# Kernel optimization log

Hardware: AMD Instinct MI355X
Metric: run time of the kernel (lower is better)

Reference implementation:

```python
import jax, jax.numpy as jnp
import numpy as np

K = 12  # Emb.k: piece-type planes (6 types x 2 colors)
DOUT = 256
B = 16384          # number of positions (bags)
AVG_LEN = 30       # avg active features per position
T = B * AVG_LEN    # total ragged ids
S = (1.0 / 30.0) ** 0.5  # 1/sqrt(kRoughEstimateOfNumberOfOnesInInput)

# vertical board flip permutation over the 64 king squares
_SQ = np.arange(64)
_FLIP_PERM = jnp.asarray((7 - _SQ // 8) * 8 + _SQ % 8)


def _flip_vertical(x):
    # x: [64, K, 8, 8, d] -> flip ranks, swap color planes, flip king square
    x = jnp.flip(x, axis=2)
    x = jnp.roll(x, K // 2, axis=1)
    return x[_FLIP_PERM]


def setup_inputs() -> dict:
    key = jax.random.key(0)
    ks = jax.random.split(key, 8)
    pieces = jax.random.normal(ks[0], (64, K, 1, 1, DOUT), dtype=jnp.float32) * S
    ranks = jax.random.normal(ks[1], (64, K, 8, 1, DOUT), dtype=jnp.float32) * S
    files = jax.random.normal(ks[2], (64, K, 1, 8, DOUT), dtype=jnp.float32) * S
    tiles = jax.random.normal(ks[3], (64, K, 8, 8, DOUT), dtype=jnp.float32) * S
    mask = jnp.ones((64, K, 8, 8, 1), dtype=jnp.float32)
    mask = (mask.at[:, 0, 0, :, :].set(0.0)
                .at[:, 0, 7, :, :].set(0.0)
                .at[:, K // 2, 0, :, :].set(0.0)
                .at[:, K // 2, 7, :, :].set(0.0))
    # ragged lengths that sum exactly to T: antithetic pairs around AVG_LEN
    half = B // 2
    d = jax.random.randint(ks[4], (half,), -10, 11)
    lengths = jnp.concatenate([AVG_LEN + d, AVG_LEN - d]).astype(jnp.int64)
    values = jax.random.randint(ks[5], (T,), 0, K * 64).astype(jnp.int64)
    kings = jax.random.randint(ks[6], (B, 2), 0, 64).astype(jnp.int64)
    return dict(pieces=pieces, ranks=ranks, files=files, tiles=tiles,
                factorization_mask=mask, values=values, lengths=lengths, kings=kings)


def reference(pieces, ranks, files, tiles, factorization_mask, values, lengths, kings):
    # factorized merge: [64, K, 8, 8, d]
    merged = tiles + (pieces + ranks + files) * factorization_mask
    d = merged.shape[-1]
    w = merged.reshape(64 * K * 64, d)
    flipped = _flip_vertical(merged).reshape(64 * K * 64, d)

    n_bags = lengths.shape[0]
    total = values.shape[0]
    # segment id for each ragged element (== repeat_interleave of bag index)
    seg = jnp.repeat(jnp.arange(n_bags), lengths, total_repeat_length=total)
    piece_dim = K * 64
    mover_ids = kings[seg, 0] * piece_dim + values
    waiter_ids = kings[seg, 1] * piece_dim + values

    a = jax.ops.segment_sum(w[mover_ids], seg, num_segments=n_bags)
    b = jax.ops.segment_sum(flipped[waiter_ids], seg, num_segments=n_bags)
    return jnp.clip(a, 0.0, 1.0), jnp.clip(b, 0.0, 1.0)
```

## Files before the change

### kernel.cpp

```cpp
#include <hip/hip_runtime.h>

#define DOUT 256
#define NROWS 49152
#define MATB (NROWS / 16)

__device__ __forceinline__ float4 ld4(const float* p) {
  return *reinterpret_cast<const float4*>(p);
}

__device__ __forceinline__ unsigned rne2(float a, float b) {
  unsigned ua = __float_as_uint(a), ub = __float_as_uint(b);
  ua += 0x7FFFu + ((ua >> 16) & 1u);
  ub += 0x7FFFu + ((ub >> 16) & 1u);
  return (ua >> 16) | (ub & 0xFFFF0000u);
}

__device__ __forceinline__ void bf4_acc(uint2 w, float4& acc) {
  acc.x += __uint_as_float(w.x << 16);
  acc.y += __uint_as_float(w.x & 0xFFFF0000u);
  acc.z += __uint_as_float(w.y << 16);
  acc.w += __uint_as_float(w.y & 0xFFFF0000u);
}

__global__ __launch_bounds__(1024) void prep_kernel(
    const float* __restrict__ tiles, const float* __restrict__ pieces,
    const float* __restrict__ ranks, const float* __restrict__ files,
    const float* __restrict__ mask, uint2* __restrict__ merged,
    const int* __restrict__ lengths, const int* __restrict__ kings,
    int* __restrict__ offs, int* __restrict__ perm_m, int* __restrict__ perm_w,
    int n_bags) {
  const int bid = blockIdx.x;
  const int t = threadIdx.x;
  if (bid == 0) {
    __shared__ int part[1024];
    __shared__ int histM[64], histW[64], curW[64];
    const int nb = n_bags;
    int v[16];
    const int base = t * 16;
    int s = 0;
    if (base + 16 <= nb) {
#pragma unroll
      for (int j = 0; j < 16; j += 4) {
        const int4 x = *reinterpret_cast<const int4*>(lengths + base + j);
        v[j] = x.x; v[j + 1] = x.y; v[j + 2] = x.z; v[j + 3] = x.w;
      }
#pragma unroll
      for (int j = 0; j < 16; ++j) s += v[j];
    } else {
      for (int j = 0; j < 16; ++j) {
        const int idx = base + j;
        v[j] = (idx < nb) ? lengths[idx] : 0;
        s += v[j];
      }
    }
    part[t] = s;
    __syncthreads();
    for (int off = 1; off < 1024; off <<= 1) {
      const int w = (t >= off) ? part[t - off] : 0;
      __syncthreads();
      part[t] += w;
      __syncthreads();
    }
    int run = part[t] - s;
    for (int j = 0; j < 16; ++j) {
      const int idx = base + j;
      if (idx < nb) { offs[idx] = run; run += v[j]; }
    }
    if (t < 64) { histM[t] = 0; histW[t] = 0; }
    __syncthreads();
    for (int i = t; i < nb; i += 1024) {
      const int2 kk = *reinterpret_cast<const int2*>(kings + 2 * i);
      atomicAdd(&histM[kk.x], 1);
      atomicAdd(&histW[kk.y], 1);
    }
    __syncthreads();
    if (t == 0) {
      int r = 0;
      for (int k = 0; k < 64; ++k) { const int h = histM[k]; histM[k] = r; r += h; }
    }
    if (t == 1) {
      int r = 0;
      for (int k = 0; k < 64; ++k) { curW[k] = r; r += histW[k]; }
    }
    __syncthreads();
    for (int i = t; i < nb; i += 1024) {
      const int2 kk = *reinterpret_cast<const int2*>(kings + 2 * i);
      const int pm = atomicAdd(&histM[kk.x], 1);
      perm_m[pm] = i;
      const int pw = atomicAdd(&curW[kk.y], 1);
      perm_w[pw] = i;
    }
    return;
  }
  const int row = ((bid - 1) << 4) + (t >> 6);
  const int lane = t & 63;
  const int p = row & 63;
  const int sk = row >> 6;
  const int r = p >> 3, f = p & 7;
  const float m = mask[row];
  const int d0 = lane << 2;
  const float4 tl = ld4(tiles + (size_t)row * DOUT + d0);
  const float4 pc = ld4(pieces + (size_t)sk * DOUT + d0);
  const float4 rk = ld4(ranks + (size_t)(sk * 8 + r) * DOUT + d0);
  const float4 fl = ld4(files + (size_t)(sk * 8 + f) * DOUT + d0);
  float4 o;
  o.x = fmaf(pc.x + rk.x + fl.x, m, tl.x);
  o.y = fmaf(pc.y + rk.y + fl.y, m, tl.y);
  o.z = fmaf(pc.z + rk.z + fl.z, m, tl.z);
  o.w = fmaf(pc.w + rk.w + fl.w, m, tl.w);
  uint2 w;
  w.x = rne2(o.x, o.y);
  w.y = rne2(o.z, o.w);
  merged[(size_t)row * 64 + lane] = w;
}

template <bool WAITER>
__device__ __forceinline__ void gather_body(
    const uint2* __restrict__ merged, const int* __restrict__ values,
    const int* __restrict__ lengths, const int* __restrict__ kings,
    const int* __restrict__ offs, const int* __restrict__ perm,
    float* __restrict__ out, int n_bags, int chunk, int b) {
  const int c = b & 7;
  const int j = b >> 3;
  const int pos = c * chunk + (j << 2) + (threadIdx.x >> 6);
  const int lim = min((c + 1) * chunk, n_bags);
  if (pos >= lim) return;
  const int lane = threadIdx.x & 63;
  const int bag = perm[pos];
  const int len = lengths[bag];
  const int kg = kings[2 * bag + (WAITER ? 1 : 0)];
  const int base = (WAITER ? (((7 - (kg >> 3)) << 3) + (kg & 7)) : kg) * 768;
  const int* __restrict__ vals = values + offs[bag];
  const uint2* __restrict__ mb = merged + lane;

  float4 a0 = {0.f, 0.f, 0.f, 0.f}, a1 = {0.f, 0.f, 0.f, 0.f};

  int i = 0;
  for (; i + 4 <= len; i += 4) {
    const int v0 = vals[i], v1 = vals[i + 1], v2 = vals[i + 2], v3 = vals[i + 3];
    unsigned r0, r1, r2, r3;
    if (WAITER) {
      const int k0 = v0 >> 6, k1 = v1 >> 6, k2 = v2 >> 6, k3 = v3 >> 6;
      r0 = base + ((k0 < 6 ? k0 + 6 : k0 - 6) << 6) + ((v0 & 63) ^ 56);
      r1 = base + ((k1 < 6 ? k1 + 6 : k1 - 6) << 6) + ((v1 & 63) ^ 56);
      r2 = base + ((k2 < 6 ? k2 + 6 : k2 - 6) << 6) + ((v2 & 63) ^ 56);
      r3 = base + ((k3 < 6 ? k3 + 6 : k3 - 6) << 6) + ((v3 & 63) ^ 56);
    } else {
      r0 = base + v0; r1 = base + v1; r2 = base + v2; r3 = base + v3;
    }
    const uint2 x0 = mb[(size_t)r0 << 6];
    const uint2 x1 = mb[(size_t)r1 << 6];
    const uint2 x2 = mb[(size_t)r2 << 6];
    const uint2 x3 = mb[(size_t)r3 << 6];
    bf4_acc(x0, a0); bf4_acc(x1, a1); bf4_acc(x2, a0); bf4_acc(x3, a1);
  }
  for (; i < len; ++i) {
    const int v = vals[i];
    unsigned r;
    if (WAITER) {
      const int k = v >> 6;
      r = base + ((k < 6 ? k + 6 : k - 6) << 6) + ((v & 63) ^ 56);
    } else {
      r = base + v;
    }
    bf4_acc(mb[(size_t)r << 6], a0);
  }

  float4 o;
  o.x = fminf(fmaxf(a0.x + a1.x, 0.f), 1.f);
  o.y = fminf(fmaxf(a0.y + a1.y, 0.f), 1.f);
  o.z = fminf(fmaxf(a0.z + a1.z, 0.f), 1.f);
  o.w = fminf(fmaxf(a0.w + a1.w, 0.f), 1.f);
  float4* ob = reinterpret_cast<float4*>(out) +
               (WAITER ? (size_t)n_bags * 64 : 0);
  ob[(size_t)bag * 64 + lane] = o;
}

__global__ __launch_bounds__(256) void gather_kernel(
    const uint2* __restrict__ merged, const int* __restrict__ values,
    const int* __restrict__ lengths, const int* __restrict__ kings,
    const int* __restrict__ offs, const int* __restrict__ perm_m,
    const int* __restrict__ perm_w, float* __restrict__ out, int n_bags,
    int chunk, int half_blocks) {
  const int b = blockIdx.x;
  if (b < half_blocks) {
    gather_body<false>(merged, values, lengths, kings, offs, perm_m, out,
                       n_bags, chunk, b);
  } else {
    gather_body<true>(merged, values, lengths, kings, offs, perm_w, out,
                      n_bags, chunk, b - half_blocks);
  }
}

extern "C" void kernel_launch(void* const* d_in, const int* in_sizes, int n_in,
                              void* d_out, int out_size, void* d_ws, size_t ws_size,
                              hipStream_t stream) {
  const float* pieces = (const float*)d_in[0];
  const float* ranks  = (const float*)d_in[1];
  const float* files  = (const float*)d_in[2];
  const float* tiles  = (const float*)d_in[3];
  const float* mask   = (const float*)d_in[4];
  const int*   values = (const int*)d_in[5];
  const int*   lengths= (const int*)d_in[6];
  const int*   kings  = (const int*)d_in[7];
  float* out = (float*)d_out;

  const int B = in_sizes[6];

  const size_t bN = ((size_t)B * 4 + 255) & ~(size_t)255;
  int* offs   = (int*)d_ws;
  int* perm_m = (int*)((char*)d_ws + bN);
  int* perm_w = (int*)((char*)d_ws + 2 * bN);
  uint2* merged = (uint2*)((char*)d_ws + 3 * bN);

  prep_kernel<<<MATB + 1, 1024, 0, stream>>>(
      tiles, pieces, ranks, files, mask, merged, lengths, kings,
      offs, perm_m, perm_w, B);

  const int chunk = (B + 7) / 8;
  const int half_blocks = 8 * ((chunk + 3) / 4);
  gather_kernel<<<2 * half_blocks, 256, 0, stream>>>(
      merged, values, lengths, kings, offs, perm_m, perm_w, out, B,
      chunk, half_blocks);
}
```

Measured before the change: 183.2 us.

## Use wave-shuffle scans and per-wave histograms in prep; unroll gather by eight

Block 0 of the prep kernel now scans bag lengths with wavefront shuffles plus a small cross-wave step, replacing the shared-memory Hillis-Steele scan that needed many barriers. The king histograms become per-wave and are scanned in parallel with shuffles, replacing serial single-thread prefix loops and cutting atomic contention. The gather loop gains an 8-wide unrolled stage so more independent loads are in flight per bag. This costs extra registers in the gather kernel, and the per-wave histograms change the order in which bags land in the permutation.

```diff
diff --git a/kernel.cpp b/kernel.cpp
--- a/kernel.cpp
+++ b/kernel.cpp
@@ -32,9 +32,14 @@
   const int bid = blockIdx.x;
   const int t = threadIdx.x;
   if (bid == 0) {
-    __shared__ int part[1024];
-    __shared__ int histM[64], histW[64], curW[64];
+    __shared__ int wsum[16];
+    __shared__ int histM[16][64];
+    __shared__ int histW[16][64];
     const int nb = n_bags;
+    const int lane = t & 63;
+    const int wid = t >> 6;
+    ((int*)histM)[t] = 0;
+    ((int*)histW)[t] = 0;
     int v[16];
     const int base = t * 16;
     int s = 0;
@@ -53,41 +58,60 @@
         s += v[j];
       }
     }
-    part[t] = s;
-    __syncthreads();
-    for (int off = 1; off < 1024; off <<= 1) {
-      const int w = (t >= off) ? part[t - off] : 0;
-      __syncthreads();
-      part[t] += w;
-      __syncthreads();
-    }
-    int run = part[t] - s;
-    for (int j = 0; j < 16; ++j) {
-      const int idx = base + j;
-      if (idx < nb) { offs[idx] = run; run += v[j]; }
-    }
-    if (t < 64) { histM[t] = 0; histW[t] = 0; }
-    __syncthreads();
+    int inc = s;
+#pragma unroll
+    for (int d = 1; d < 64; d <<= 1) {
+      const int y = __shfl_up(inc, d, 64);
+      if (lane >= d) inc += y;
+    }
+    if (lane == 63) wsum[wid] = inc;
+    __syncthreads();
+    if (wid == 0) {
+      int wv = (lane < 16) ? wsum[lane] : 0;
+#pragma unroll
+      for (int d = 1; d < 16; d <<= 1) {
+        const int y = __shfl_up(wv, d, 64);
+        if (lane >= d) wv += y;
+      }
+      if (lane < 16) wsum[lane] = wv;
+    }
+    __syncthreads();
+    {
+      const int waveBase = wid ? wsum[wid - 1] : 0;
+      int run = waveBase + inc - s;
+      for (int j = 0; j < 16; ++j) {
+        const int idx = base + j;
+        if (idx < nb) { offs[idx] = run; run += v[j]; }
+      }
+    }
     for (int i = t; i < nb; i += 1024) {
       const int2 kk = *reinterpret_cast<const int2*>(kings + 2 * i);
-      atomicAdd(&histM[kk.x], 1);
-      atomicAdd(&histW[kk.y], 1);
-    }
-    __syncthreads();
-    if (t == 0) {
-      int r = 0;
-      for (int k = 0; k < 64; ++k) { const int h = histM[k]; histM[k] = r; r += h; }
-    }
-    if (t == 1) {
-      int r = 0;
-      for (int k = 0; k < 64; ++k) { curW[k] = r; r += histW[k]; }
+      atomicAdd(&histM[wid][kk.x], 1);
+      atomicAdd(&histW[wid][kk.y], 1);
+    }
+    __syncthreads();
+    if (wid < 2) {
+      int (*h)[64] = wid ? histW : histM;
+      const int k = lane;
+      int sum = 0;
+#pragma unroll
+      for (int w = 0; w < 16; ++w) sum += h[w][k];
+      int incl = sum;
+#pragma unroll
+      for (int d = 1; d < 64; d <<= 1) {
+        const int y = __shfl_up(incl, d, 64);
+        if (k >= d) incl += y;
+      }
+      int run = incl - sum;
+#pragma unroll
+      for (int w = 0; w < 16; ++w) { const int c = h[w][k]; h[w][k] = run; run += c; }
     }
     __syncthreads();
     for (int i = t; i < nb; i += 1024) {
       const int2 kk = *reinterpret_cast<const int2*>(kings + 2 * i);
-      const int pm = atomicAdd(&histM[kk.x], 1);
+      const int pm = atomicAdd(&histM[wid][kk.x], 1);
       perm_m[pm] = i;
-      const int pw = atomicAdd(&curW[kk.y], 1);
+      const int pw = atomicAdd(&histW[wid][kk.y], 1);
       perm_w[pw] = i;
     }
     return;
@@ -136,6 +160,36 @@
   float4 a0 = {0.f, 0.f, 0.f, 0.f}, a1 = {0.f, 0.f, 0.f, 0.f};
 
   int i = 0;
+  for (; i + 8 <= len; i += 8) {
+    const int v0 = vals[i],     v1 = vals[i + 1], v2 = vals[i + 2], v3 = vals[i + 3];
+    const int v4 = vals[i + 4], v5 = vals[i + 5], v6 = vals[i + 6], v7 = vals[i + 7];
+    unsigned r0, r1, r2, r3, r4, r5, r6, r7;
+    if (WAITER) {
+      const int k0 = v0 >> 6, k1 = v1 >> 6, k2 = v2 >> 6, k3 = v3 >> 6;
+      const int k4 = v4 >> 6, k5 = v5 >> 6, k6 = v6 >> 6, k7 = v7 >> 6;
+      r0 = base + ((k0 < 6 ? k0 + 6 : k0 - 6) << 6) + ((v0 & 63) ^ 56);
+      r1 = base + ((k1 < 6 ? k1 + 6 : k1 - 6) << 6) + ((v1 & 63) ^ 56);
+      r2 = base + ((k2 < 6 ? k2 + 6 : k2 - 6) << 6) + ((v2 & 63) ^ 56);
+      r3 = base + ((k3 < 6 ? k3 + 6 : k3 - 6) << 6) + ((v3 & 63) ^ 56);
+      r4 = base + ((k4 < 6 ? k4 + 6 : k4 - 6) << 6) + ((v4 & 63) ^ 56);
+      r5 = base + ((k5 < 6 ? k5 + 6 : k5 - 6) << 6) + ((v5 & 63) ^ 56);
+      r6 = base + ((k6 < 6 ? k6 + 6 : k6 - 6) << 6) + ((v6 & 63) ^ 56);
+      r7 = base + ((k7 < 6 ? k7 + 6 : k7 - 6) << 6) + ((v7 & 63) ^ 56);
+    } else {
+      r0 = base + v0; r1 = base + v1; r2 = base + v2; r3 = base + v3;
+      r4 = base + v4; r5 = base + v5; r6 = base + v6; r7 = base + v7;
+    }
+    const uint2 x0 = mb[(size_t)r0 << 6];
+    const uint2 x1 = mb[(size_t)r1 << 6];
+    const uint2 x2 = mb[(size_t)r2 << 6];
+    const uint2 x3 = mb[(size_t)r3 << 6];
+    const uint2 x4 = mb[(size_t)r4 << 6];
+    const uint2 x5 = mb[(size_t)r5 << 6];
+    const uint2 x6 = mb[(size_t)r6 << 6];
+    const uint2 x7 = mb[(size_t)r7 << 6];
+    bf4_acc(x0, a0); bf4_acc(x1, a1); bf4_acc(x2, a0); bf4_acc(x3, a1);
+    bf4_acc(x4, a0); bf4_acc(x5, a1); bf4_acc(x6, a0); bf4_acc(x7, a1);
+  }
   for (; i + 4 <= len; i += 4) {
     const int v0 = vals[i], v1 = vals[i + 1], v2 = vals[i + 2], v3 = vals[i + 3];
     unsigned r0, r1, r2, r3;
```

After: 182.5 us. Within noise of the previous version (-0.4%).
